# Kernel optimization log

Measured on AMD Instinct MI355X. Metric: run time of the kernel, lower is better.

## Reference

```python
import jax, jax.numpy as jnp
import numpy as np

T, B, E, H = 2048, 2, 1024, 16

def setup_inputs() -> dict:
    rng = jax.random.key(0)
    ks = jax.random.split(rng, 7)
    s = 0.02
    return {
        "query": jax.random.normal(ks[0], (T, B, E), jnp.float32),
        "key": jax.random.normal(ks[1], (T, B, E), jnp.float32),
        "value": jax.random.normal(ks[2], (T, B, E), jnp.float32),
        "in_proj_weight": jax.random.normal(ks[3], (3 * E, E), jnp.float32) * s,
        "in_proj_bias": jax.random.normal(ks[4], (3 * E,), jnp.float32) * s,
        "out_proj_weight": jax.random.normal(ks[5], (E, E), jnp.float32) * s,
        "out_proj_bias": jax.random.normal(ks[6], (E,), jnp.float32) * s,
    }

def reference(query, key, value, in_proj_weight, in_proj_bias, out_proj_weight, out_proj_bias):
    tgt_len, bsz, embed_dim = query.shape
    num_heads = H
    head_dim = embed_dim // num_heads
    scaling = head_dim ** -0.5
    wq, wk, wv = jnp.split(in_proj_weight, 3, axis=0)
    bq, bk, bv = jnp.split(in_proj_bias, 3, axis=0)
    # projections: F.linear(x, W, b) = x @ W.T + b
    q = (query @ wq.T + bq) * scaling          # (T, B, E)
    k = key @ wk.T + bk                        # (S, B, E)
    v = value @ wv.T + bv                      # (S, B, E)
    # (len, B, E) -> (B*H, len, head_dim), matching torch view+transpose
    def to_heads(x):
        L = x.shape[0]
        return x.reshape(L, bsz * num_heads, head_dim).transpose(1, 0, 2)
    q, k, v = to_heads(q), to_heads(k), to_heads(v)
    scores = jnp.einsum('bqd,bkd->bqk', q, k)  # (B*H, T, S)
    attn = jax.nn.softmax(scores, axis=-1)
    out = jnp.einsum('bqk,bkd->bqd', attn, v)  # (B*H, T, head_dim)
    out = out.transpose(1, 0, 2).reshape(tgt_len, bsz, embed_dim)
    out = out @ out_proj_weight.T + out_proj_bias
    return out
```

## Files before the change

kernel.cpp:

```cpp
#include <hip/hip_runtime.h>
#include <cstdint>
#include <cstddef>

#define QSCALE 0.18033688011112042f

typedef __attribute__((ext_vector_type(8))) short bf16x8;
typedef __attribute__((ext_vector_type(4))) float f32x4;

#define MFMA(a, b, c) __builtin_amdgcn_mfma_f32_16x16x32_bf16(a, b, c, 0, 0, 0)

#define PIPE_SYNC() do {                                   \
    asm volatile("s_waitcnt vmcnt(0)" ::: "memory");       \
    __builtin_amdgcn_sched_barrier(0);                     \
    __builtin_amdgcn_s_barrier();                          \
    __builtin_amdgcn_sched_barrier(0);                     \
  } while (0)

typedef union { unsigned int u[4]; bf16x8 b; } pku;

__device__ __forceinline__ unsigned short cvt_bf16(float x) {
  union { float f; unsigned int u; } v;
  v.f = x;
  unsigned int r = v.u + 0x7FFFu + ((v.u >> 16) & 1u);
  return (unsigned short)(r >> 16);
}

__device__ __forceinline__ void gll16(const void* g, void* l) {
  __builtin_amdgcn_global_load_lds(
      (const __attribute__((address_space(1))) unsigned int*)g,
      (__attribute__((address_space(3))) unsigned int*)l, 16, 0, 0);
}

__device__ __forceinline__ float fast_exp2(float x) {
#if __has_builtin(__builtin_amdgcn_exp2f)
  return __builtin_amdgcn_exp2f(x);
#else
  float r; asm("v_exp_f32 %0, %1" : "=v"(r) : "v"(x)); return r;
#endif
}

__device__ __forceinline__ unsigned int pack_bf16(float lo, float hi) {
  union { float f; unsigned int u; } a, b;
  a.f = lo; b.f = hi;
  return __builtin_amdgcn_perm(b.u + 0x8000u, a.u + 0x8000u, 0x07060302u);
}

__global__ void cvt_all(const float* __restrict__ q,
                        const float* __restrict__ k,
                        const float* __restrict__ v,
                        const float* __restrict__ ipw,
                        const float* __restrict__ opw,
                        unsigned short* __restrict__ dst) {
  const size_t i = ((size_t)blockIdx.x * 256 + threadIdx.x) * 8;
  const float* src;
  float scale = 1.0f;
  if (i < 4194304) src = q + i;
  else if (i < 8388608) src = k + (i - 4194304);
  else if (i < 12582912) src = v + (i - 8388608);
  else {
    const size_t w = i - 12582912;
    if (w < 3145728) { src = ipw + w; if (w < 1048576) scale = QSCALE; }
    else src = opw + (w - 3145728);
  }
  float4 a = *(const float4*)src;
  float4 b = *(const float4*)(src + 4);
  uint4 o;
  o.x = cvt_bf16(a.x * scale) | ((unsigned int)cvt_bf16(a.y * scale) << 16);
  o.y = cvt_bf16(a.z * scale) | ((unsigned int)cvt_bf16(a.w * scale) << 16);
  o.z = cvt_bf16(b.x * scale) | ((unsigned int)cvt_bf16(b.y * scale) << 16);
  o.w = cvt_bf16(b.z * scale) | ((unsigned int)cvt_bf16(b.w * scale) << 16);
  *(uint4*)(dst + i) = o;
}

__global__ __launch_bounds__(256, 3) void gemm_qkv(
    const unsigned short* __restrict__ X,
    const unsigned short* __restrict__ W,
    const float* __restrict__ bias,
    unsigned short* __restrict__ Qh,
    unsigned short* __restrict__ Kh,
    unsigned short* __restrict__ Vt)
{
  __shared__ unsigned short As[128 * 64];
  __shared__ unsigned short Bs[128 * 64];
  const int tid = threadIdx.x;
  const int wave = tid >> 6, lane = tid & 63;
  const int quad = lane >> 4, l16 = lane & 15;
  const int flat = blockIdx.x + (blockIdx.y << 3) + (blockIdx.z << 8);
  const int nf = (flat & 7) * 96 + (flat >> 3);
  const int z = nf >> 8;
  const int m0 = ((nf >> 3) & 31) * 128;
  const int n0 = (nf & 7) * 128;
  const unsigned short* Ab = X + (size_t)z * 4194304 + (size_t)m0 * 1024;
  const unsigned short* Bb = W + ((size_t)z * 1024 + n0) * 1024;
  const int wr = (wave >> 1) * 64, wc = (wave & 1) * 64;

  const f32x4 z4 = {0.f, 0.f, 0.f, 0.f};
  f32x4 acc[4][4];
#pragma unroll
  for (int i = 0; i < 4; ++i)
#pragma unroll
    for (int j = 0; j < 4; ++j) acc[i][j] = z4;

  for (int k0 = 0; k0 < 1024; k0 += 64) {
    __syncthreads();
#pragma unroll
    for (int j = 0; j < 4; ++j) {
      const int c = j * 256 + tid;
      const int row = c >> 3, pc = c & 7;
      const int kc = pc ^ (row & 7);
      gll16(Ab + (size_t)row * 1024 + k0 + kc * 8, &As[c * 8]);
      gll16(Bb + (size_t)row * 1024 + k0 + kc * 8, &Bs[c * 8]);
    }
    __syncthreads();
#pragma unroll
    for (int kk = 0; kk < 2; ++kk) {
      bf16x8 af[4], bfr[4];
#pragma unroll
      for (int rt = 0; rt < 4; ++rt) {
        const int row = wr + rt * 16 + l16;
        af[rt] = *(const bf16x8*)&As[row * 64 + ((kk * 4 + quad) ^ (row & 7)) * 8];
      }
#pragma unroll
      for (int ct = 0; ct < 4; ++ct) {
        const int row = wc + ct * 16 + l16;
        bfr[ct] = *(const bf16x8*)&Bs[row * 64 + ((kk * 4 + quad) ^ (row & 7)) * 8];
      }
#pragma unroll
      for (int rt = 0; rt < 4; ++rt)
#pragma unroll
        for (int ct = 0; ct < 4; ++ct)
          acc[rt][ct] = MFMA(af[rt], bfr[ct], acc[rt][ct]);
    }
  }

#pragma unroll
  for (int rt = 0; rt < 4; ++rt)
#pragma unroll
    for (int ct = 0; ct < 4; ++ct) {
      const int gn = n0 + wc + ct * 16 + l16;
      float bv = bias[z * 1024 + gn];
      if (z == 0) bv *= QSCALE;
      const int h = gn >> 6, d = gn & 63;
#pragma unroll
      for (int r = 0; r < 4; ++r) {
        const int gm = m0 + wr + rt * 16 + quad * 4 + r;
        const int t = gm >> 1, b = gm & 1;
        const int bh = b * 16 + h;
        const unsigned short o = cvt_bf16(acc[rt][ct][r] + bv);
        if (z == 0)      Qh[((size_t)bh * 2048 + t) * 64 + d] = o;
        else if (z == 1) Kh[((size_t)bh * 2048 + t) * 64 + d] = o;
        else {
          const int w32 = t & 31;
          const int tp = (t & ~31) | (((w32 >> 2) & 3) << 3) | ((w32 >> 4) << 2) | (w32 & 3);
          Vt[((size_t)bh * 64 + d) * 2048 + tp] = o;
        }
      }
    }
}

__global__ __launch_bounds__(256, 2) void attn(
    const unsigned short* __restrict__ Qh,
    const unsigned short* __restrict__ Kh,
    const unsigned short* __restrict__ Vt,
    unsigned short* __restrict__ O)
{
  __shared__ unsigned short KV[2][16384];
  __shared__ float Ls[128];
  const int tid = threadIdx.x;
  const int wave = tid >> 6, lane = tid & 63;
  const int quad = lane >> 4, l16 = lane & 15;
  const int pair = wave >> 1, kh = wave & 1;
  const int flat = blockIdx.x + (blockIdx.y << 4);
  const int nf = (flat & 7) * 64 + (flat >> 3);
  const int qt = nf & 15, bh = nf >> 4;
  const unsigned short* Qb = Qh + ((size_t)bh * 2048 + qt * 128 + pair * 64) * 64;
  const unsigned short* Kb = Kh + (size_t)bh * 2048 * 64;
  const unsigned short* Vb = Vt + (size_t)bh * 64 * 2048;

  bf16x8 qf[4][2];
#pragma unroll
  for (int g = 0; g < 4; ++g)
#pragma unroll
    for (int kk = 0; kk < 2; ++kk)
      qf[g][kk] = *(const bf16x8*)(Qb + (size_t)(g * 16 + l16) * 64 + kk * 32 + quad * 8);

  const unsigned short* kp[4];
  const unsigned short* vp[4];
  int klo[4], vlo[4];
#pragma unroll
  for (int j = 0; j < 4; ++j) {
    const int c = wave * 256 + j * 64 + lane;
    const int r = c >> 3, cc = c & 7;
    kp[j] = Kb + (size_t)r * 64 + (cc ^ (r & 7)) * 8;
    klo[j] = c * 8;
    const int r2 = c >> 4, cc2 = c & 15;
    vp[j] = Vb + (size_t)r2 * 2048 + (cc2 ^ (r2 & 15)) * 8;
    vlo[j] = 8192 + c * 8;
  }

  pku ones;
  ones.u[0] = ones.u[1] = ones.u[2] = ones.u[3] = 0x3F803F80u;

  const f32x4 z4 = {0.f, 0.f, 0.f, 0.f};
  f32x4 oacc[4][4];
  f32x4 lacc[4] = {z4, z4, z4, z4};
#pragma unroll
  for (int g = 0; g < 4; ++g)
#pragma unroll
    for (int c = 0; c < 4; ++c) oacc[g][c] = z4;

#pragma unroll
  for (int j = 0; j < 4; ++j) {
    gll16(kp[j], &KV[0][klo[j]]);
    gll16(vp[j], &KV[0][vlo[j]]);
    kp[j] += 128 * 64;
    vp[j] += 128;
  }

#pragma unroll 1
  for (int it = 0; it < 16; ++it) {
    const int cur = it & 1;
    PIPE_SYNC();
    if (it < 15) {
#pragma unroll
      for (int j = 0; j < 4; ++j) {
        gll16(kp[j], &KV[cur ^ 1][klo[j]]);
        gll16(vp[j], &KV[cur ^ 1][vlo[j]]);
        kp[j] += 128 * 64;
        vp[j] += 128;
      }
    }
    const unsigned short* Ks = KV[cur];
    const unsigned short* Vs = KV[cur] + 8192;

#pragma unroll
    for (int jj = 0; jj < 2; ++jj) {
      unsigned int pk0[4][2], pk1[4][2];
#pragma unroll
      for (int half = 0; half < 2; ++half) {
        const int ct = jj * 2 + half;
        const int R = kh * 64 + ct * 16 + l16;
        bf16x8 kfr[2];
#pragma unroll
        for (int kk = 0; kk < 2; ++kk)
          kfr[kk] = *(const bf16x8*)&Ks[R * 64 + ((kk * 4 + quad) ^ (R & 7)) * 8];
#pragma unroll
        for (int g = 0; g < 4; ++g) {
          f32x4 sv = z4;
          sv = MFMA(kfr[0], qf[g][0], sv);
          sv = MFMA(kfr[1], qf[g][1], sv);
          f32x4 p;
#pragma unroll
          for (int r = 0; r < 4; ++r) p[r] = fast_exp2(sv[r]);
          pk0[g][half] = pack_bf16(p[0], p[1]);
          pk1[g][half] = pack_bf16(p[2], p[3]);
        }
      }
      const int jjg = kh * 2 + jj;
      __builtin_amdgcn_s_setprio(1);
#pragma unroll
      for (int ctd = 0; ctd < 4; ++ctd) {
        const int R = ctd * 16 + l16;
        const int phys = (jjg * 4 + quad) ^ (R & 15);
        const bf16x8 vv = *(const bf16x8*)&Vs[R * 128 + phys * 8];
#pragma unroll
        for (int g = 0; g < 4; ++g) {
          pku a;
          a.u[0] = pk0[g][0]; a.u[1] = pk1[g][0];
          a.u[2] = pk0[g][1]; a.u[3] = pk1[g][1];
          oacc[g][ctd] = MFMA(a.b, vv, oacc[g][ctd]);
        }
      }
#pragma unroll
      for (int g = 0; g < 4; ++g) {
        pku a;
        a.u[0] = pk0[g][0]; a.u[1] = pk1[g][0];
        a.u[2] = pk0[g][1]; a.u[3] = pk1[g][1];
        lacc[g] = MFMA(a.b, ones.b, lacc[g]);
      }
      __builtin_amdgcn_s_setprio(0);
    }
  }

  __syncthreads();
  float* Fp = (float*)KV;
  if (kh == 1) {
#pragma unroll
    for (int g = 0; g < 4; ++g) {
#pragma unroll
      for (int ctd = 0; ctd < 4; ++ctd)
#pragma unroll
        for (int r = 0; r < 4; ++r)
          Fp[pair * 4224 + (g * 16 + quad * 4 + r) * 66 + ctd * 16 + l16] = oacc[g][ctd][r];
      if (l16 == 0) {
#pragma unroll
        for (int r = 0; r < 4; ++r)
          Ls[pair * 64 + g * 16 + quad * 4 + r] = lacc[g][r];
      }
    }
  }
  __syncthreads();
  if (kh == 0) {
    const int b = bh >> 4, h = bh & 15;
#pragma unroll
    for (int g = 0; g < 4; ++g)
#pragma unroll
      for (int r = 0; r < 4; ++r) {
        const int ql = g * 16 + quad * 4 + r;
        const float lv = lacc[g][r] + Ls[pair * 64 + ql];
        const float inv = 1.0f / lv;
        const int t = qt * 128 + pair * 64 + ql;
#pragma unroll
        for (int ctd = 0; ctd < 4; ++ctd) {
          const float val = oacc[g][ctd][r] + Fp[pair * 4224 + ql * 66 + ctd * 16 + l16];
          O[((size_t)t * 2 + b) * 1024 + h * 64 + ctd * 16 + l16] = cvt_bf16(val * inv);
        }
      }
  }
}

__global__ __launch_bounds__(256, 4) void gemm_out(
    const unsigned short* __restrict__ A,
    const unsigned short* __restrict__ W,
    const float* __restrict__ bias,
    float* __restrict__ out)
{
  __shared__ unsigned short As[128 * 64];
  __shared__ unsigned short Bs[64 * 64];
  const int tid = threadIdx.x;
  const int wave = tid >> 6, lane = tid & 63;
  const int quad = lane >> 4, l16 = lane & 15;
  const int flat = blockIdx.x + (blockIdx.y << 4);
  const int nf = (flat & 7) * 64 + (flat >> 3);
  const int m0 = (nf >> 4) * 128;
  const int n0 = (nf & 15) * 64;
  const unsigned short* Ab = A + (size_t)m0 * 1024;
  const unsigned short* Bb = W + (size_t)n0 * 1024;
  const int wr = (wave >> 1) * 64, wc = (wave & 1) * 32;

  const f32x4 z4 = {0.f, 0.f, 0.f, 0.f};
  f32x4 acc[4][2];
#pragma unroll
  for (int i = 0; i < 4; ++i)
#pragma unroll
    for (int j = 0; j < 2; ++j) acc[i][j] = z4;

  for (int k0 = 0; k0 < 1024; k0 += 64) {
    __syncthreads();
#pragma unroll
    for (int j = 0; j < 4; ++j) {
      const int c = j * 256 + tid;
      const int row = c >> 3, pc = c & 7;
      const int kc = pc ^ (row & 7);
      gll16(Ab + (size_t)row * 1024 + k0 + kc * 8, &As[c * 8]);
    }
#pragma unroll
    for (int j = 0; j < 2; ++j) {
      const int c = j * 256 + tid;
      const int row = c >> 3, pc = c & 7;
      const int kc = pc ^ (row & 7);
      gll16(Bb + (size_t)row * 1024 + k0 + kc * 8, &Bs[c * 8]);
    }
    __syncthreads();
#pragma unroll
    for (int kk = 0; kk < 2; ++kk) {
      bf16x8 af[4], bfr[2];
#pragma unroll
      for (int rt = 0; rt < 4; ++rt) {
        const int row = wr + rt * 16 + l16;
        af[rt] = *(const bf16x8*)&As[row * 64 + ((kk * 4 + quad) ^ (row & 7)) * 8];
      }
#pragma unroll
      for (int ct = 0; ct < 2; ++ct) {
        const int row = wc + ct * 16 + l16;
        bfr[ct] = *(const bf16x8*)&Bs[row * 64 + ((kk * 4 + quad) ^ (row & 7)) * 8];
      }
#pragma unroll
      for (int rt = 0; rt < 4; ++rt)
#pragma unroll
        for (int ct = 0; ct < 2; ++ct)
          acc[rt][ct] = MFMA(af[rt], bfr[ct], acc[rt][ct]);
    }
  }

#pragma unroll
  for (int rt = 0; rt < 4; ++rt)
#pragma unroll
    for (int ct = 0; ct < 2; ++ct) {
      const int gn = n0 + wc + ct * 16 + l16;
      const float bv = bias[gn];
#pragma unroll
      for (int r = 0; r < 4; ++r) {
        const int gm = m0 + wr + rt * 16 + quad * 4 + r;
        out[(size_t)gm * 1024 + gn] = acc[rt][ct][r] + bv;
      }
    }
}

extern "C" void kernel_launch(void* const* d_in, const int* in_sizes, int n_in,
                              void* d_out, int out_size, void* d_ws, size_t ws_size,
                              hipStream_t stream) {
  const float* q   = (const float*)d_in[0];
  const float* k   = (const float*)d_in[1];
  const float* v   = (const float*)d_in[2];
  const float* ipw = (const float*)d_in[3];
  const float* ipb = (const float*)d_in[4];
  const float* opw = (const float*)d_in[5];
  const float* opb = (const float*)d_in[6];

  unsigned short* ws = (unsigned short*)d_ws;
  unsigned short* X  = ws;
  unsigned short* Wb = ws + 12582912;
  unsigned short* Wo = ws + 15728640;
  unsigned short* Qh = ws + 16777216;
  unsigned short* Kh = ws + 20971520;
  unsigned short* Vx = ws + 25165824;
  unsigned short* Oa = ws + 29360128;

  cvt_all<<<dim3(8192), 256, 0, stream>>>(q, k, v, ipw, opw, ws);
  gemm_qkv<<<dim3(8, 32, 3), 256, 0, stream>>>(X, Wb, ipb, Qh, Kh, Vx);
  attn<<<dim3(16, 32), 256, 0, stream>>>(Qh, Kh, Vx, Oa);
  gemm_out<<<dim3(16, 32), 256, 0, stream>>>(Oa, Wo, opb, (float*)d_out);
}
```

Measured before the change: 210.5 us.

## Split attention key tiles across four waves per query group with tree reduction

The attention kernel now runs 512 threads per block: each 64-row query group gets four waves, and each wave handles a 32-key quarter of every 128-key tile instead of two waves taking halves. Partial output and row-sum accumulators are combined through shared memory in a two-step tree reduction. The aim is more waves per CU to hide MFMA and LDS latency, and fewer loads per thread for K/V staging. The cost is extra reduction barriers and shared-memory traffic, plus higher register pressure under launch_bounds(512,4).

```diff
diff --git a/kernel.cpp b/kernel.cpp
--- a/kernel.cpp
+++ b/kernel.cpp
@@ -158,22 +158,22 @@
     }
 }
 
-__global__ __launch_bounds__(256, 2) void attn(
+__global__ __launch_bounds__(512, 4) void attn(
     const unsigned short* __restrict__ Qh,
     const unsigned short* __restrict__ Kh,
     const unsigned short* __restrict__ Vt,
     unsigned short* __restrict__ O)
 {
   __shared__ unsigned short KV[2][16384];
-  __shared__ float Ls[128];
+  __shared__ float Ls2[2][3][64];
   const int tid = threadIdx.x;
   const int wave = tid >> 6, lane = tid & 63;
   const int quad = lane >> 4, l16 = lane & 15;
-  const int pair = wave >> 1, kh = wave & 1;
+  const int qg = wave >> 2, kq = wave & 3;
   const int flat = blockIdx.x + (blockIdx.y << 4);
   const int nf = (flat & 7) * 64 + (flat >> 3);
   const int qt = nf & 15, bh = nf >> 4;
-  const unsigned short* Qb = Qh + ((size_t)bh * 2048 + qt * 128 + pair * 64) * 64;
+  const unsigned short* Qb = Qh + ((size_t)bh * 2048 + qt * 128 + qg * 64) * 64;
   const unsigned short* Kb = Kh + (size_t)bh * 2048 * 64;
   const unsigned short* Vb = Vt + (size_t)bh * 64 * 2048;
 
@@ -184,12 +184,12 @@
     for (int kk = 0; kk < 2; ++kk)
       qf[g][kk] = *(const bf16x8*)(Qb + (size_t)(g * 16 + l16) * 64 + kk * 32 + quad * 8);
 
-  const unsigned short* kp[4];
-  const unsigned short* vp[4];
-  int klo[4], vlo[4];
-#pragma unroll
-  for (int j = 0; j < 4; ++j) {
-    const int c = wave * 256 + j * 64 + lane;
+  const unsigned short* kp[2];
+  const unsigned short* vp[2];
+  int klo[2], vlo[2];
+#pragma unroll
+  for (int j = 0; j < 2; ++j) {
+    const int c = j * 512 + tid;
     const int r = c >> 3, cc = c & 7;
     kp[j] = Kb + (size_t)r * 64 + (cc ^ (r & 7)) * 8;
     klo[j] = c * 8;
@@ -210,7 +210,7 @@
     for (int c = 0; c < 4; ++c) oacc[g][c] = z4;
 
 #pragma unroll
-  for (int j = 0; j < 4; ++j) {
+  for (int j = 0; j < 2; ++j) {
     gll16(kp[j], &KV[0][klo[j]]);
     gll16(vp[j], &KV[0][vlo[j]]);
     kp[j] += 128 * 64;
@@ -223,7 +223,7 @@
     PIPE_SYNC();
     if (it < 15) {
 #pragma unroll
-      for (int j = 0; j < 4; ++j) {
+      for (int j = 0; j < 2; ++j) {
         gll16(kp[j], &KV[cur ^ 1][klo[j]]);
         gll16(vp[j], &KV[cur ^ 1][vlo[j]]);
         kp[j] += 128 * 64;
@@ -233,86 +233,106 @@
     const unsigned short* Ks = KV[cur];
     const unsigned short* Vs = KV[cur] + 8192;
 
-#pragma unroll
-    for (int jj = 0; jj < 2; ++jj) {
-      unsigned int pk0[4][2], pk1[4][2];
-#pragma unroll
-      for (int half = 0; half < 2; ++half) {
-        const int ct = jj * 2 + half;
-        const int R = kh * 64 + ct * 16 + l16;
-        bf16x8 kfr[2];
-#pragma unroll
-        for (int kk = 0; kk < 2; ++kk)
-          kfr[kk] = *(const bf16x8*)&Ks[R * 64 + ((kk * 4 + quad) ^ (R & 7)) * 8];
-#pragma unroll
-        for (int g = 0; g < 4; ++g) {
-          f32x4 sv = z4;
-          sv = MFMA(kfr[0], qf[g][0], sv);
-          sv = MFMA(kfr[1], qf[g][1], sv);
-          f32x4 p;
-#pragma unroll
-          for (int r = 0; r < 4; ++r) p[r] = fast_exp2(sv[r]);
-          pk0[g][half] = pack_bf16(p[0], p[1]);
-          pk1[g][half] = pack_bf16(p[2], p[3]);
-        }
-      }
-      const int jjg = kh * 2 + jj;
-      __builtin_amdgcn_s_setprio(1);
-#pragma unroll
-      for (int ctd = 0; ctd < 4; ++ctd) {
-        const int R = ctd * 16 + l16;
-        const int phys = (jjg * 4 + quad) ^ (R & 15);
-        const bf16x8 vv = *(const bf16x8*)&Vs[R * 128 + phys * 8];
-#pragma unroll
-        for (int g = 0; g < 4; ++g) {
-          pku a;
-          a.u[0] = pk0[g][0]; a.u[1] = pk1[g][0];
-          a.u[2] = pk0[g][1]; a.u[3] = pk1[g][1];
-          oacc[g][ctd] = MFMA(a.b, vv, oacc[g][ctd]);
-        }
-      }
+    unsigned int pk0[4][2], pk1[4][2];
+#pragma unroll
+    for (int half = 0; half < 2; ++half) {
+      const int R = kq * 32 + half * 16 + l16;
+      bf16x8 kfr[2];
+#pragma unroll
+      for (int kk = 0; kk < 2; ++kk)
+        kfr[kk] = *(const bf16x8*)&Ks[R * 64 + ((kk * 4 + quad) ^ (R & 7)) * 8];
+#pragma unroll
+      for (int g = 0; g < 4; ++g) {
+        f32x4 sv = z4;
+        sv = MFMA(kfr[0], qf[g][0], sv);
+        sv = MFMA(kfr[1], qf[g][1], sv);
+        f32x4 p;
+#pragma unroll
+        for (int r = 0; r < 4; ++r) p[r] = fast_exp2(sv[r]);
+        pk0[g][half] = pack_bf16(p[0], p[1]);
+        pk1[g][half] = pack_bf16(p[2], p[3]);
+      }
+    }
+    __builtin_amdgcn_s_setprio(1);
+#pragma unroll
+    for (int ctd = 0; ctd < 4; ++ctd) {
+      const int R = ctd * 16 + l16;
+      const int phys = (kq * 4 + quad) ^ (R & 15);
+      const bf16x8 vv = *(const bf16x8*)&Vs[R * 128 + phys * 8];
 #pragma unroll
       for (int g = 0; g < 4; ++g) {
         pku a;
         a.u[0] = pk0[g][0]; a.u[1] = pk1[g][0];
         a.u[2] = pk0[g][1]; a.u[3] = pk1[g][1];
-        lacc[g] = MFMA(a.b, ones.b, lacc[g]);
-      }
-      __builtin_amdgcn_s_setprio(0);
-    }
-  }
-
+        oacc[g][ctd] = MFMA(a.b, vv, oacc[g][ctd]);
+      }
+    }
+#pragma unroll
+    for (int g = 0; g < 4; ++g) {
+      pku a;
+      a.u[0] = pk0[g][0]; a.u[1] = pk1[g][0];
+      a.u[2] = pk0[g][1]; a.u[3] = pk1[g][1];
+      lacc[g] = MFMA(a.b, ones.b, lacc[g]);
+    }
+    __builtin_amdgcn_s_setprio(0);
+  }
+
+  float* Fp = (float*)KV;
   __syncthreads();
-  float* Fp = (float*)KV;
-  if (kh == 1) {
-#pragma unroll
-    for (int g = 0; g < 4; ++g) {
+  if (kq == 1 || kq == 3) {
+    const int base = (qg * 2 + (kq >> 1)) * 4096;
+#pragma unroll
+    for (int g = 0; g < 4; ++g)
 #pragma unroll
       for (int ctd = 0; ctd < 4; ++ctd)
 #pragma unroll
         for (int r = 0; r < 4; ++r)
-          Fp[pair * 4224 + (g * 16 + quad * 4 + r) * 66 + ctd * 16 + l16] = oacc[g][ctd][r];
-      if (l16 == 0) {
+          Fp[base + (g * 16 + quad * 4 + r) * 64 + ctd * 16 + l16] = oacc[g][ctd][r];
+  }
+  if (kq != 0 && l16 == 0) {
+#pragma unroll
+    for (int g = 0; g < 4; ++g)
+#pragma unroll
+      for (int r = 0; r < 4; ++r)
+        Ls2[qg][kq - 1][g * 16 + quad * 4 + r] = lacc[g][r];
+  }
+  __syncthreads();
+  if (kq == 0 || kq == 2) {
+    const int base = (qg * 2 + (kq >> 1)) * 4096;
+#pragma unroll
+    for (int g = 0; g < 4; ++g)
+#pragma unroll
+      for (int ctd = 0; ctd < 4; ++ctd)
 #pragma unroll
         for (int r = 0; r < 4; ++r)
-          Ls[pair * 64 + g * 16 + quad * 4 + r] = lacc[g][r];
-      }
-    }
+          oacc[g][ctd][r] += Fp[base + (g * 16 + quad * 4 + r) * 64 + ctd * 16 + l16];
   }
   __syncthreads();
-  if (kh == 0) {
+  if (kq == 2) {
+    const int base = qg * 4096;
+#pragma unroll
+    for (int g = 0; g < 4; ++g)
+#pragma unroll
+      for (int ctd = 0; ctd < 4; ++ctd)
+#pragma unroll
+        for (int r = 0; r < 4; ++r)
+          Fp[base + (g * 16 + quad * 4 + r) * 64 + ctd * 16 + l16] = oacc[g][ctd][r];
+  }
+  __syncthreads();
+  if (kq == 0) {
     const int b = bh >> 4, h = bh & 15;
+    const int base = qg * 4096;
 #pragma unroll
     for (int g = 0; g < 4; ++g)
 #pragma unroll
       for (int r = 0; r < 4; ++r) {
         const int ql = g * 16 + quad * 4 + r;
-        const float lv = lacc[g][r] + Ls[pair * 64 + ql];
+        const float lv = lacc[g][r] + Ls2[qg][0][ql] + Ls2[qg][1][ql] + Ls2[qg][2][ql];
         const float inv = 1.0f / lv;
-        const int t = qt * 128 + pair * 64 + ql;
+        const int t = qt * 128 + qg * 64 + ql;
 #pragma unroll
         for (int ctd = 0; ctd < 4; ++ctd) {
-          const float val = oacc[g][ctd][r] + Fp[pair * 4224 + ql * 66 + ctd * 16 + l16];
+          const float val = oacc[g][ctd][r] + Fp[base + ql * 64 + ctd * 16 + l16];
           O[((size_t)t * 2 + b) * 1024 + h * 64 + ctd * 16 + l16] = cvt_bf16(val * inv);
         }
       }
@@ -419,6 +439,6 @@
 
   cvt_all<<<dim3(8192), 256, 0, stream>>>(q, k, v, ipw, opw, ws);
   gemm_qkv<<<dim3(8, 32, 3), 256, 0, stream>>>(X, Wb, ipb, Qh, Kh, Vx);
-  attn<<<dim3(16, 32), 256, 0, stream>>>(Qh, Kh, Vx, Oa);
+  attn<<<dim3(16, 32), 512, 0, stream>>>(Qh, Kh, Vx, Oa);
   gemm_out<<<dim3(16, 32), 256, 0, stream>>>(Oa, Wo, opb, (float*)d_out);
 }
```

Result: slower. 376.1 us (+78.7%).
